# Kernel optimization log

Measured on AMD Instinct MI355X. Metric: run time of the kernel, lower is better.

The kernel has to match this reference:

```python
import jax, jax.numpy as jnp
import numpy as np

EMBED_DIM = 1024
NUM_HEADS = 16
HEAD_DIM = EMBED_DIM // NUM_HEADS


def setup_inputs() -> dict:
    key = jax.random.key(0)
    k1, k2, k3, k4, k5 = jax.random.split(key, 5)
    B, N, C = 4, 2048, EMBED_DIM
    s = 1.0 / np.sqrt(C)
    return {
        "x": jax.random.normal(k1, (B, N, C), dtype=jnp.float32),
        "w_qkv": jax.random.uniform(k2, (C, 3 * C), dtype=jnp.float32, minval=-s, maxval=s),
        "b_qkv": jax.random.uniform(k3, (3 * C,), dtype=jnp.float32, minval=-s, maxval=s),
        "w_out": jax.random.uniform(k4, (C, C), dtype=jnp.float32, minval=-s, maxval=s),
        "b_out": jax.random.uniform(k5, (C,), dtype=jnp.float32, minval=-s, maxval=s),
    }


def reference(x, w_qkv, b_qkv, w_out, b_out):
    B, N, C = x.shape
    H, D = NUM_HEADS, HEAD_DIM
    qkv = x @ w_qkv + b_qkv                       # [B, N, 3C]
    qkv = qkv.reshape(B, N, 3, H, D)
    q = qkv[:, :, 0].transpose(0, 2, 1, 3)        # [B, H, N, D]
    k = qkv[:, :, 1].transpose(0, 2, 1, 3)
    v = qkv[:, :, 2].transpose(0, 2, 1, 3)
    scale = 1.0 / np.sqrt(D).astype(np.float32)
    attn = jnp.einsum('bhnd,bhmd->bhnm', q, k) * scale  # [B, H, N, N]
    attn = jax.nn.softmax(attn, axis=-1)
    out = jnp.einsum('bhnm,bhmd->bhnd', attn, v)  # [B, H, N, D]
    out = out.transpose(0, 2, 1, 3).reshape(B, N, C)
    return out @ w_out + b_out
```

## Files before the change

kernel.cpp:

```cpp
#include <hip/hip_runtime.h>


typedef unsigned short u16;
typedef unsigned long long u64;
typedef __bf16 bf16x8 __attribute__((ext_vector_type(8)));
typedef float f32x4 __attribute__((ext_vector_type(4)));

#define MFMA(a, b, c) __builtin_amdgcn_mfma_f32_16x16x32_bf16(a, b, c, 0, 0, 0)

__device__ __forceinline__ u16 f2bf(float f) {
    __bf16 h = (__bf16)f;
    return *(u16*)&h;
}

__device__ __forceinline__ void gld16(const void* g, void* l) {
    __builtin_amdgcn_global_load_lds(
        (const __attribute__((address_space(1))) void*)g,
        (__attribute__((address_space(3))) void*)l, 16, 0, 0);
}

__device__ __forceinline__ void lds_fence_wave() {
    __asm__ volatile("s_waitcnt lgkmcnt(0)" ::: "memory");
}

__global__ __launch_bounds__(256) void cvt_f32_bf16(
    const float* __restrict__ src, u16* __restrict__ dst, long n)
{
    long i = ((long)blockIdx.x * 256 + threadIdx.x) * 8;
    if (i >= n) return;
    float4 a = *(const float4*)&src[i];
    float4 b = *(const float4*)&src[i + 4];
    union { u16 u[8]; uint4 v; } tmp;
    tmp.u[0] = f2bf(a.x); tmp.u[1] = f2bf(a.y);
    tmp.u[2] = f2bf(a.z); tmp.u[3] = f2bf(a.w);
    tmp.u[4] = f2bf(b.x); tmp.u[5] = f2bf(b.y);
    tmp.u[6] = f2bf(b.z); tmp.u[7] = f2bf(b.w);
    *(uint4*)&dst[i] = tmp.v;
}

__global__ __launch_bounds__(256) void transpose_f2b(
    const float* __restrict__ src, u16* __restrict__ dst, int R, int C)
{
    __shared__ alignas(16) u16 tile[64 * 80];
    const int r0 = blockIdx.y * 64, c0 = blockIdx.x * 64;
    const int t = threadIdx.x;
#pragma unroll
    for (int c = 0; c < 4; c++) {
        int idx = t + c * 256;
        int r = idx >> 4, seg = idx & 15;
        float4 f = *(const float4*)&src[(long)(r0 + r) * C + c0 + seg * 4];
        u16* p = &tile[r * 80 + seg * 4];
        p[0] = f2bf(f.x); p[1] = f2bf(f.y); p[2] = f2bf(f.z); p[3] = f2bf(f.w);
    }
    __syncthreads();
#pragma unroll
    for (int c = 0; c < 2; c++) {
        int idx = t + c * 256;
        int rr = idx >> 3, seg = idx & 7;
        union { u16 u[8]; uint4 v; } tmp;
#pragma unroll
        for (int j = 0; j < 8; j++) tmp.u[j] = tile[(seg * 8 + j) * 80 + rr];
        *(uint4*)&dst[(long)(c0 + rr) * R + r0 + seg * 8] = tmp.v;
    }
}

template <int EPI>
__global__ __launch_bounds__(256) void gemm_bf16(
    const u16* __restrict__ A, const u16* __restrict__ Bt,
    const float* __restrict__ bias,
    u16* __restrict__ out0, u16* __restrict__ out1, u16* __restrict__ out2,
    float* __restrict__ outf,
    int M, int N, int K)
{
    const int m0 = blockIdx.x * 128, n0 = blockIdx.y * 128;
    const int t = threadIdx.x;
    const int wave = t >> 6, lane = t & 63, quad = lane >> 4, l15 = lane & 15;
    const int wm = wave >> 1, wn = wave & 1;

    __shared__ alignas(16) u16 As[128 * 64];
    __shared__ alignas(16) u16 Bs[128 * 64];

    const int srow = wave * 32 + (lane >> 3);
    const int scol = (((lane & 7) ^ (lane >> 3)) & 7) * 8;

    f32x4 acc[4][4] = {};

    for (int k0 = 0; k0 < K; k0 += 64) {
        __syncthreads();
#pragma unroll
        for (int c = 0; c < 4; c++) {
            gld16(&A[(long)(m0 + srow + c * 8) * K + k0 + scol],
                  &As[(wave * 32 + c * 8) * 64]);
            gld16(&Bt[(long)(n0 + srow + c * 8) * K + k0 + scol],
                  &Bs[(wave * 32 + c * 8) * 64]);
        }
        __syncthreads();

#pragma unroll
        for (int ks = 0; ks < 2; ks++) {
            bf16x8 af[4], bf[4];
#pragma unroll
            for (int mt = 0; mt < 4; mt++) {
                int row = wm * 64 + mt * 16 + l15;
                af[mt] = *(bf16x8*)&As[row * 64 + (((ks * 4 + quad) ^ (row & 7)) * 8)];
            }
#pragma unroll
            for (int nt = 0; nt < 4; nt++) {
                int row = wn * 64 + nt * 16 + l15;
                bf[nt] = *(bf16x8*)&Bs[row * 64 + (((ks * 4 + quad) ^ (row & 7)) * 8)];
            }
#pragma unroll
            for (int mt = 0; mt < 4; mt++)
#pragma unroll
                for (int nt = 0; nt < 4; nt++)
                    acc[mt][nt] = MFMA(bf[nt], af[mt], acc[mt][nt]);
        }
    }

#pragma unroll
    for (int mt = 0; mt < 4; mt++) {
        int token = m0 + wm * 64 + mt * 16 + l15;
        int bb = token >> 11, nn = token & 2047;
#pragma unroll
        for (int nt = 0; nt < 4; nt++) {
            int cgb = n0 + wn * 64 + nt * 16 + quad * 4;
            float4 bv = *(const float4*)&bias[cgb];
            float v0 = acc[mt][nt][0] + bv.x;
            float v1 = acc[mt][nt][1] + bv.y;
            float v2 = acc[mt][nt][2] + bv.z;
            float v3 = acc[mt][nt][3] + bv.w;
            if (EPI == 0) {
                int t3 = cgb >> 10;
                int hh = (cgb >> 6) & 15, dd = cgb & 63;
                int bh = (bb << 4) + hh;
                if (t3 == 0) {
                    union { u16 u[4]; u64 v; } pk;
                    pk.u[0] = f2bf(v0 * 0.125f); pk.u[1] = f2bf(v1 * 0.125f);
                    pk.u[2] = f2bf(v2 * 0.125f); pk.u[3] = f2bf(v3 * 0.125f);
                    *(u64*)&out0[((long)bh * 2048 + nn) * 64 + dd] = pk.v;
                } else if (t3 == 1) {
                    union { u16 u[4]; u64 v; } pk;
                    pk.u[0] = f2bf(v0); pk.u[1] = f2bf(v1);
                    pk.u[2] = f2bf(v2); pk.u[3] = f2bf(v3);
                    *(u64*)&out1[((long)bh * 2048 + nn) * 64 + dd] = pk.v;
                } else {
                    long vbo = ((long)bh * 64 + dd) * 2048 + nn;
                    out2[vbo]            = f2bf(v0);
                    out2[vbo + 2048]     = f2bf(v1);
                    out2[vbo + 2 * 2048] = f2bf(v2);
                    out2[vbo + 3 * 2048] = f2bf(v3);
                }
            } else {
                float4 o4 = { v0, v1, v2, v3 };
                *(float4*)&outf[(long)token * N + cgb] = o4;
            }
        }
    }
}

__global__ __launch_bounds__(256, 3) void flash_attn(
    const u16* __restrict__ q, const u16* __restrict__ k,
    const u16* __restrict__ vt, u16* __restrict__ attn)
{
    const int bh = blockIdx.y;
    const int b = bh >> 4, h = bh & 15;
    const int q0 = blockIdx.x * 128;
    const int t = threadIdx.x;
    const int wave = t >> 6, lane = t & 63, quad = lane >> 4, l15 = lane & 15;

    __shared__ alignas(16) u16 Ks[2][4096];
    __shared__ alignas(16) u16 Vs[2][4096];
    __shared__ alignas(16) __bf16 Ps[128 * 72];

    const u16* kb = k + (long)bh * 2048 * 64;
    const u16* vb = vt + (long)bh * 64 * 2048;

    bf16x8 qf[2][2];
#pragma unroll
    for (int mt = 0; mt < 2; mt++) {
        long row = (long)bh * 2048 + q0 + wave * 32 + mt * 16 + l15;
        qf[mt][0] = *(const bf16x8*)&q[row * 64 + quad * 8];
        qf[mt][1] = *(const bf16x8*)&q[row * 64 + 32 + quad * 8];
    }

    bf16x8 ones;
#pragma unroll
    for (int j = 0; j < 8; j++) ones[j] = (__bf16)1.0f;

    const int ri = lane >> 3;
    const int ci = (lane & 7) ^ ri;
    const int s0 = wave * 2;

    const int sw0 = ((quad ^ (l15 & 7)) * 8);
    const int prow = (wave * 32 + l15) * 72;

    f32x4 o[2][4] = {};
    f32x4 ls[2] = {};

#pragma unroll
    for (int c = 0; c < 2; c++) {
        int s = s0 + c;
        gld16(&kb[(long)(s * 8 + ri) * 64 + ci * 8], &Ks[0][s * 512]);
        gld16(&vb[(long)(s * 8 + ri) * 2048 + ci * 8], &Vs[0][s * 512]);
    }

    for (int kt = 0; kt < 32; kt++) {
        const int cur = kt & 1;
        __syncthreads();

        if (kt < 31) {
#pragma unroll
            for (int c = 0; c < 2; c++) {
                int s = s0 + c;
                gld16(&kb[(long)((kt + 1) * 64 + s * 8 + ri) * 64 + ci * 8],
                      &Ks[cur ^ 1][s * 512]);
                gld16(&vb[(long)(s * 8 + ri) * 2048 + (kt + 1) * 64 + ci * 8],
                      &Vs[cur ^ 1][s * 512]);
            }
        }

        f32x4 st[2][4];
#pragma unroll
        for (int ct = 0; ct < 4; ct++) {
            const u16* kr = &Ks[cur][(ct * 16 + l15) * 64];
            bf16x8 kf0 = *(const bf16x8*)&kr[sw0];
            bf16x8 kf1 = *(const bf16x8*)&kr[sw0 ^ 32];
#pragma unroll
            for (int mt = 0; mt < 2; mt++) {
                f32x4 z = {};
                z = MFMA(kf0, qf[mt][0], z);
                st[mt][ct] = MFMA(kf1, qf[mt][1], z);
            }
        }

#pragma unroll
        for (int mt = 0; mt < 2; mt++)
#pragma unroll
            for (int ct = 0; ct < 4; ct++) {
                union { u16 u[4]; u64 v; } pk;
#pragma unroll
                for (int r = 0; r < 4; r++)
                    pk.u[r] = f2bf(__expf(st[mt][ct][r]));
                *(u64*)&Ps[prow + mt * 16 * 72 + ct * 16 + quad * 4] = pk.v;
            }
        lds_fence_wave();

        bf16x8 pb[2][2];
#pragma unroll
        for (int mt = 0; mt < 2; mt++) {
            pb[mt][0] = *(bf16x8*)&Ps[prow + mt * 16 * 72 + quad * 8];
            pb[mt][1] = *(bf16x8*)&Ps[prow + mt * 16 * 72 + 32 + quad * 8];
            ls[mt] = MFMA(ones, pb[mt][0], ls[mt]);
            ls[mt] = MFMA(ones, pb[mt][1], ls[mt]);
        }
#pragma unroll
        for (int dt = 0; dt < 4; dt++) {
            const u16* vr = &Vs[cur][(dt * 16 + l15) * 64];
            bf16x8 va0 = *(const bf16x8*)&vr[sw0];
            bf16x8 va1 = *(const bf16x8*)&vr[sw0 ^ 32];
#pragma unroll
            for (int mt = 0; mt < 2; mt++) {
                o[mt][dt] = MFMA(va0, pb[mt][0], o[mt][dt]);
                o[mt][dt] = MFMA(va1, pb[mt][1], o[mt][dt]);
            }
        }
    }

#pragma unroll
    for (int mt = 0; mt < 2; mt++) {
        float inv = 1.f / ls[mt][0];
        int n = q0 + wave * 32 + mt * 16 + l15;
#pragma unroll
        for (int dt = 0; dt < 4; dt++) {
            union { u16 u[4]; u64 v; } pk;
#pragma unroll
            for (int r = 0; r < 4; r++) pk.u[r] = f2bf(o[mt][dt][r] * inv);
            *(u64*)&attn[((long)b * 2048 + n) * 1024 + h * 64 + dt * 16 + quad * 4] =
                pk.v;
        }
    }
}

extern "C" void kernel_launch(void* const* d_in, const int* in_sizes, int n_in,
                              void* d_out, int out_size, void* d_ws, size_t ws_size,
                              hipStream_t stream) {
    const float* x     = (const float*)d_in[0];
    const float* w_qkv = (const float*)d_in[1];
    const float* b_qkv = (const float*)d_in[2];
    const float* w_out = (const float*)d_in[3];
    const float* b_out = (const float*)d_in[4];
    float* out = (float*)d_out;

    u16* ws    = (u16*)d_ws;
    u16* q     = ws;
    u16* kk    = q + 8388608;
    u16* vt    = kk + 8388608;
    u16* attn  = vt + 8388608;
    u16* x_bf  = attn + 8388608;
    u16* wqkvT = x_bf + 8388608;
    u16* woutT = wqkvT + 3145728;

    cvt_f32_bf16<<<4096, 256, 0, stream>>>(x, x_bf, 8388608L);
    transpose_f2b<<<dim3(48, 16), 256, 0, stream>>>(w_qkv, wqkvT, 1024, 3072);
    transpose_f2b<<<dim3(16, 16), 256, 0, stream>>>(w_out, woutT, 1024, 1024);
    gemm_bf16<0><<<dim3(64, 24), 256, 0, stream>>>(x_bf, wqkvT, b_qkv, q, kk, vt,
                                                   nullptr, 8192, 3072, 1024);
    flash_attn<<<dim3(16, 64), 256, 0, stream>>>(q, kk, vt, attn);
    gemm_bf16<1><<<dim3(64, 8), 256, 0, stream>>>(attn, woutT, b_out, nullptr,
                                                  nullptr, nullptr, out,
                                                  8192, 1024, 1024);
}
```

Before: 292.1 us.

## Use 32x32x16 MFMA in flash attention with register-shuffled P instead of LDS

Switches the attention inner loops from 16x16x32 MFMA tiles to 32x32x16 tiles. The P matrix is now passed between the QK and PV products through cross-lane shuffles rather than a round trip through an LDS buffer. Row sums are accumulated with scalar adds plus one shuffle instead of MFMAs against a ones vector. The log2(e) factor is folded into the Q scale so exp2f can replace __expf, and occupancy is raised to 4 blocks per SM. Removing the P buffer frees LDS, but the change adds shuffle traffic and register pressure under the tighter launch bound.

```diff
diff --git a/kernel.cpp b/kernel.cpp
--- a/kernel.cpp
+++ b/kernel.cpp
@@ -5,8 +5,12 @@
 typedef unsigned long long u64;
 typedef __bf16 bf16x8 __attribute__((ext_vector_type(8)));
 typedef float f32x4 __attribute__((ext_vector_type(4)));
+typedef float f32x16 __attribute__((ext_vector_type(16)));
 
 #define MFMA(a, b, c) __builtin_amdgcn_mfma_f32_16x16x32_bf16(a, b, c, 0, 0, 0)
+#define MFMA32(a, b, c) __builtin_amdgcn_mfma_f32_32x32x16_bf16(a, b, c, 0, 0, 0)
+
+#define QSCALE 0.18033688011112042f
 
 __device__ __forceinline__ u16 f2bf(float f) {
     __bf16 h = (__bf16)f;
@@ -17,10 +21,6 @@
     __builtin_amdgcn_global_load_lds(
         (const __attribute__((address_space(1))) void*)g,
         (__attribute__((address_space(3))) void*)l, 16, 0, 0);
-}
-
-__device__ __forceinline__ void lds_fence_wave() {
-    __asm__ volatile("s_waitcnt lgkmcnt(0)" ::: "memory");
 }
 
 __global__ __launch_bounds__(256) void cvt_f32_bf16(
@@ -135,8 +135,8 @@
                 int bh = (bb << 4) + hh;
                 if (t3 == 0) {
                     union { u16 u[4]; u64 v; } pk;
-                    pk.u[0] = f2bf(v0 * 0.125f); pk.u[1] = f2bf(v1 * 0.125f);
-                    pk.u[2] = f2bf(v2 * 0.125f); pk.u[3] = f2bf(v3 * 0.125f);
+                    pk.u[0] = f2bf(v0 * QSCALE); pk.u[1] = f2bf(v1 * QSCALE);
+                    pk.u[2] = f2bf(v2 * QSCALE); pk.u[3] = f2bf(v3 * QSCALE);
                     *(u64*)&out0[((long)bh * 2048 + nn) * 64 + dd] = pk.v;
                 } else if (t3 == 1) {
                     union { u16 u[4]; u64 v; } pk;
@@ -158,7 +158,7 @@
     }
 }
 
-__global__ __launch_bounds__(256, 3) void flash_attn(
+__global__ __launch_bounds__(256, 4) void flash_attn(
     const u16* __restrict__ q, const u16* __restrict__ k,
     const u16* __restrict__ vt, u16* __restrict__ attn)
 {
@@ -166,36 +166,29 @@
     const int b = bh >> 4, h = bh & 15;
     const int q0 = blockIdx.x * 128;
     const int t = threadIdx.x;
-    const int wave = t >> 6, lane = t & 63, quad = lane >> 4, l15 = lane & 15;
+    const int wave = t >> 6, lane = t & 63;
+    const int l31 = lane & 31, h1 = lane >> 5;
 
     __shared__ alignas(16) u16 Ks[2][4096];
     __shared__ alignas(16) u16 Vs[2][4096];
-    __shared__ alignas(16) __bf16 Ps[128 * 72];
 
     const u16* kb = k + (long)bh * 2048 * 64;
     const u16* vb = vt + (long)bh * 64 * 2048;
 
-    bf16x8 qf[2][2];
-#pragma unroll
-    for (int mt = 0; mt < 2; mt++) {
-        long row = (long)bh * 2048 + q0 + wave * 32 + mt * 16 + l15;
-        qf[mt][0] = *(const bf16x8*)&q[row * 64 + quad * 8];
-        qf[mt][1] = *(const bf16x8*)&q[row * 64 + 32 + quad * 8];
-    }
-
-    bf16x8 ones;
-#pragma unroll
-    for (int j = 0; j < 8; j++) ones[j] = (__bf16)1.0f;
+    bf16x8 qf[4];
+    {
+        long row = (long)bh * 2048 + q0 + wave * 32 + l31;
+#pragma unroll
+        for (int dc = 0; dc < 4; dc++)
+            qf[dc] = *(const bf16x8*)&q[row * 64 + dc * 16 + h1 * 8];
+    }
 
     const int ri = lane >> 3;
     const int ci = (lane & 7) ^ ri;
     const int s0 = wave * 2;
 
-    const int sw0 = ((quad ^ (l15 & 7)) * 8);
-    const int prow = (wave * 32 + l15) * 72;
-
-    f32x4 o[2][4] = {};
-    f32x4 ls[2] = {};
+    f32x16 o[2] = {};
+    float ls = 0.f;
 
 #pragma unroll
     for (int c = 0; c < 2; c++) {
@@ -219,66 +212,69 @@
             }
         }
 
-        f32x4 st[2][4];
-#pragma unroll
-        for (int ct = 0; ct < 4; ct++) {
-            const u16* kr = &Ks[cur][(ct * 16 + l15) * 64];
-            bf16x8 kf0 = *(const bf16x8*)&kr[sw0];
-            bf16x8 kf1 = *(const bf16x8*)&kr[sw0 ^ 32];
-#pragma unroll
-            for (int mt = 0; mt < 2; mt++) {
-                f32x4 z = {};
-                z = MFMA(kf0, qf[mt][0], z);
-                st[mt][ct] = MFMA(kf1, qf[mt][1], z);
-            }
-        }
-
-#pragma unroll
-        for (int mt = 0; mt < 2; mt++)
-#pragma unroll
-            for (int ct = 0; ct < 4; ct++) {
+        f32x16 s2[2];
+        s2[0] = (f32x16)0.0f;
+        s2[1] = (f32x16)0.0f;
+#pragma unroll
+        for (int kblk = 0; kblk < 2; kblk++) {
+            int row = kblk * 32 + l31;
+            const u16* kr = &Ks[cur][row * 64];
+            int rm = row & 7;
+#pragma unroll
+            for (int dc = 0; dc < 4; dc++) {
+                bf16x8 kf = *(const bf16x8*)&kr[(((2 * dc + h1) ^ rm) * 8)];
+                s2[kblk] = MFMA32(kf, qf[dc], s2[kblk]);
+            }
+        }
+
+        u64 U[8];
+        float part = 0.f;
+#pragma unroll
+        for (int kblk = 0; kblk < 2; kblk++)
+#pragma unroll
+            for (int rb = 0; rb < 4; rb++) {
                 union { u16 u[4]; u64 v; } pk;
 #pragma unroll
-                for (int r = 0; r < 4; r++)
-                    pk.u[r] = f2bf(__expf(st[mt][ct][r]));
-                *(u64*)&Ps[prow + mt * 16 * 72 + ct * 16 + quad * 4] = pk.v;
-            }
-        lds_fence_wave();
-
-        bf16x8 pb[2][2];
-#pragma unroll
-        for (int mt = 0; mt < 2; mt++) {
-            pb[mt][0] = *(bf16x8*)&Ps[prow + mt * 16 * 72 + quad * 8];
-            pb[mt][1] = *(bf16x8*)&Ps[prow + mt * 16 * 72 + 32 + quad * 8];
-            ls[mt] = MFMA(ones, pb[mt][0], ls[mt]);
-            ls[mt] = MFMA(ones, pb[mt][1], ls[mt]);
-        }
-#pragma unroll
-        for (int dt = 0; dt < 4; dt++) {
-            const u16* vr = &Vs[cur][(dt * 16 + l15) * 64];
-            bf16x8 va0 = *(const bf16x8*)&vr[sw0];
-            bf16x8 va1 = *(const bf16x8*)&vr[sw0 ^ 32];
-#pragma unroll
-            for (int mt = 0; mt < 2; mt++) {
-                o[mt][dt] = MFMA(va0, pb[mt][0], o[mt][dt]);
-                o[mt][dt] = MFMA(va1, pb[mt][1], o[mt][dt]);
-            }
-        }
-    }
-
-#pragma unroll
-    for (int mt = 0; mt < 2; mt++) {
-        float inv = 1.f / ls[mt][0];
-        int n = q0 + wave * 32 + mt * 16 + l15;
-#pragma unroll
-        for (int dt = 0; dt < 4; dt++) {
+                for (int rr = 0; rr < 4; rr++) {
+                    float e = exp2f(s2[kblk][rb * 4 + rr]);
+                    part += e;
+                    pk.u[rr] = f2bf(e);
+                }
+                U[kblk * 4 + rb] = pk.v;
+            }
+        ls += part + __shfl_xor(part, 32);
+
+#pragma unroll
+        for (int kc = 0; kc < 4; kc++) {
+            int base = (kc >> 1) * 4 + (kc & 1) * 2;
+            u64 send = U[base + (h1 ^ 1)];
+            u64 recv = __shfl_xor(send, 32);
+            union { u64 d[2]; bf16x8 v; } pf;
+            pf.d[0] = h1 ? recv : U[base];
+            pf.d[1] = h1 ? U[base + 1] : recv;
+#pragma unroll
+            for (int dblk = 0; dblk < 2; dblk++) {
+                int row = dblk * 32 + l31;
+                const u16* vr = &Vs[cur][row * 64];
+                bf16x8 vf = *(const bf16x8*)&vr[(((2 * kc + h1) ^ (row & 7)) * 8)];
+                o[dblk] = MFMA32(vf, pf.v, o[dblk]);
+            }
+        }
+    }
+
+    float inv = 1.f / ls;
+    int n = q0 + wave * 32 + l31;
+#pragma unroll
+    for (int dblk = 0; dblk < 2; dblk++)
+#pragma unroll
+        for (int rb = 0; rb < 4; rb++) {
             union { u16 u[4]; u64 v; } pk;
 #pragma unroll
-            for (int r = 0; r < 4; r++) pk.u[r] = f2bf(o[mt][dt][r] * inv);
-            *(u64*)&attn[((long)b * 2048 + n) * 1024 + h * 64 + dt * 16 + quad * 4] =
-                pk.v;
-        }
-    }
+            for (int rr = 0; rr < 4; rr++)
+                pk.u[rr] = f2bf(o[dblk][rb * 4 + rr] * inv);
+            *(u64*)&attn[((long)b * 2048 + n) * 1024 + h * 64 +
+                         dblk * 32 + rb * 8 + h1 * 4] = pk.v;
+        }
 }
 
 extern "C" void kernel_launch(void* const* d_in, const int* in_sizes, int n_in,
```

New measurement: 335.0 us. 1.15x slower.
